# Kernel tuning notes

Measured on AMD Instinct MI355X. Metric: run time of the kernel, lower is better.

Reference implementation:

```python
import jax, jax.numpy as jnp
import numpy as np

EPS = 1e-5
N, A, CTX, H, E = 100000, 32, 5, 64, 1600000


def layer_norm(x, g, b):
    mu = x.mean(-1, keepdims=True)
    var = x.var(-1, keepdims=True)
    return (x - mu) / jnp.sqrt(var + EPS) * g + b


def batch_norm(x, g, b, m, v):
    # eval-mode BatchNorm with running stats
    return (x - m) / jnp.sqrt(v + EPS) * g + b


def gcn_conv(x, w, bias, src, dst, n):
    # src/dst already include self-loops; symmetric normalization D^-1/2 (A+I) D^-1/2
    h = x @ w
    deg = jax.ops.segment_sum(jnp.ones_like(src, dtype=x.dtype), dst, num_segments=n)
    inv_sqrt = jnp.where(deg > 0, 1.0 / jnp.sqrt(deg), 0.0)
    coef = inv_sqrt[src] * inv_sqrt[dst]  # [Etot]
    return jax.ops.segment_sum(h[src] * coef[:, None], dst, num_segments=n) + bias


def gat_conv(x, w, a_src, a_dst, bias, src, dst, n, heads, out_ch):
    h = (x @ w).reshape(n, heads, out_ch)           # [N,H,C]
    alpha_s = (h * a_src).sum(-1)                    # [N,H]
    alpha_d = (h * a_dst).sum(-1)                    # [N,H]
    e = jax.nn.leaky_relu(alpha_s[src] + alpha_d[dst], 0.2)  # [Etot,H]
    m = jax.ops.segment_max(e, dst, num_segments=n)  # segment softmax over incoming edges
    ex = jnp.exp(e - m[dst])
    s = jax.ops.segment_sum(ex, dst, num_segments=n)
    alpha = ex / (s[dst] + 1e-16)                    # [Etot,H]
    out = jax.ops.segment_sum(h[src] * alpha[..., None], dst, num_segments=n)
    return out.reshape(n, heads * out_ch) + bias


def setup_inputs() -> dict:
    key = jax.random.key(0)
    ks = iter(jax.random.split(key, 48))

    def rn(shape, scale=None):
        if scale is None:  # xavier-normal-ish
            fan_in, fan_out = (shape[0], shape[-1]) if len(shape) > 1 else (shape[0], shape[0])
            scale = float(np.sqrt(2.0 / (fan_in + fan_out)))
        return jax.random.normal(next(ks), shape, jnp.float32) * scale

    inp = {
        "accessibility_features": jax.random.normal(next(ks), (N, A), jnp.float32),
        "context_features": jax.random.normal(next(ks), (N, CTX), jnp.float32),
        "edge_index": jax.random.randint(next(ks), (2, E), 0, N, jnp.int32),
        # context gate
        "cg_w1": rn((CTX, 32)), "cg_b1": jnp.zeros((32,), jnp.float32),
        "cg_w2": rn((32, 32)), "cg_b2": jnp.zeros((32,), jnp.float32),
        "cg_aw": rn((32, A)), "cg_ab": jnp.zeros((A,), jnp.float32),
        "base_imp": jnp.ones((A,), jnp.float32),
        # input LayerNorm
        "ln_g": jnp.ones((A,), jnp.float32), "ln_b": jnp.zeros((A,), jnp.float32),
        # feature encoder
        "fe_w1": rn((A, H)), "fe_b1": jnp.zeros((H,), jnp.float32),
        "fe_w2": rn((H, H)), "fe_b2": jnp.zeros((H,), jnp.float32),
        # GCN1 + BN1
        "gcn1_w": rn((H, H)), "gcn1_b": jnp.zeros((H,), jnp.float32),
        "bn1_g": 1.0 + rn((H,), 0.05), "bn1_b": rn((H,), 0.05),
        "bn1_m": rn((H,), 0.05), "bn1_v": 1.0 + jax.random.uniform(next(ks), (H,), jnp.float32) * 0.1,
        # GAT (heads=2, out=32) + BN2
        "gat_w": rn((H, H)), "gat_asrc": rn((2, 32), 0.1), "gat_adst": rn((2, 32), 0.1),
        "gat_b": jnp.zeros((H,), jnp.float32),
        "bn2_g": 1.0 + rn((H,), 0.05), "bn2_b": rn((H,), 0.05),
        "bn2_m": rn((H,), 0.05), "bn2_v": 1.0 + jax.random.uniform(next(ks), (H,), jnp.float32) * 0.1,
        # GCN2 + BN3
        "gcn2_w": rn((H, H // 2)), "gcn2_b": jnp.zeros((H // 2,), jnp.float32),
        "bn3_g": 1.0 + rn((H // 2,), 0.05), "bn3_b": rn((H // 2,), 0.05),
        "bn3_m": rn((H // 2,), 0.05), "bn3_v": 1.0 + jax.random.uniform(next(ks), (H // 2,), jnp.float32) * 0.1,
        # SVI predictor head
        "sp_w1": rn((H // 2, H // 4)), "sp_b1": jnp.zeros((H // 4,), jnp.float32),
        "sp_w2": rn((H // 4, 1)), "sp_b2": jnp.zeros((1,), jnp.float32),
    }
    return inp


def reference(accessibility_features, context_features, edge_index,
              cg_w1, cg_b1, cg_w2, cg_b2, cg_aw, cg_ab, base_imp,
              ln_g, ln_b, fe_w1, fe_b1, fe_w2, fe_b2,
              gcn1_w, gcn1_b, bn1_g, bn1_b, bn1_m, bn1_v,
              gat_w, gat_asrc, gat_adst, gat_b, bn2_g, bn2_b, bn2_m, bn2_v,
              gcn2_w, gcn2_b, bn3_g, bn3_b, bn3_m, bn3_v,
              sp_w1, sp_b1, sp_w2, sp_b2):
    n = accessibility_features.shape[0]
    loops = jnp.arange(n, dtype=edge_index.dtype)
    src = jnp.concatenate([edge_index[0], loops])
    dst = jnp.concatenate([edge_index[1], loops])

    # context-gated feature modulation
    ce = jax.nn.relu(context_features @ cg_w1 + cg_b1) @ cg_w2 + cg_b2
    attw = jax.nn.softmax(ce @ cg_aw + cg_ab, axis=-1)
    x = layer_norm(accessibility_features * (attw * base_imp), ln_g, ln_b)

    # dense feature encoder (dropout = identity in eval)
    x = jax.nn.relu(jax.nn.relu(x @ fe_w1 + fe_b1) @ fe_w2 + fe_b2)

    x = jax.nn.relu(batch_norm(gcn_conv(x, gcn1_w, gcn1_b, src, dst, n), bn1_g, bn1_b, bn1_m, bn1_v))
    x = jax.nn.relu(batch_norm(gat_conv(x, gat_w, gat_asrc, gat_adst, gat_b, src, dst, n, 2, 32), bn2_g, bn2_b, bn2_m, bn2_v))
    x = jax.nn.relu(batch_norm(gcn_conv(x, gcn2_w, gcn2_b, src, dst, n), bn3_g, bn3_b, bn3_m, bn3_v))

    svi = jax.nn.sigmoid((jax.nn.relu(x @ sp_w1 + sp_b1) @ sp_w2 + sp_b2).squeeze(-1))
    return svi
```

## Files before the change

### kernel.cpp

```cpp
#include <hip/hip_runtime.h>
#include <hip/hip_bf16.h>

constexpr int A_DIM = 32;
constexpr int CTX_DIM = 5;
constexpr float EPS = 1e-5f;
constexpr int BCAP = 4096;

__device__ __forceinline__ float lrelu02(float x) { return x > 0.f ? x : 0.2f * x; }

__device__ __forceinline__ unsigned int f2bf_bits(float x) {
    __hip_bfloat16 h = __float2bfloat16(x);
    return (unsigned int)reinterpret_cast<unsigned short&>(h);
}
__device__ __forceinline__ float bf_lo(unsigned int v) { return __uint_as_float(v << 16); }
__device__ __forceinline__ float bf_hi(unsigned int v) { return __uint_as_float(v & 0xffff0000u); }

__global__ void k_bucketA(const int* __restrict__ ei, int E, int* __restrict__ bcnt,
                          int* __restrict__ bstage) {
    int i = blockIdx.x * blockDim.x + threadIdx.x;
    int e4 = E >> 2;
    const int4* s4 = (const int4*)ei;
    const int4* d4 = (const int4*)(ei + E);
    auto put = [&](int s, int d) {
        int b = d >> 7;
        int pos = atomicAdd(&bcnt[b * 16], 1);
        if (pos < BCAP) bstage[(size_t)b * BCAP + pos] = ((d & 127) << 17) | s;
    };
    if (i < e4) {
        int4 s = s4[i];
        int4 d = d4[i];
        put(s.x, d.x);
        put(s.y, d.y);
        put(s.z, d.z);
        put(s.w, d.w);
    }
    int tb = e4 << 2;
    if (i < E - tb) put(ei[tb + i], ei[E + tb + i]);
}

__global__ void k_bscan(const int* __restrict__ bcnt, int nb, int* __restrict__ bbase,
                        int* __restrict__ rowp, int n, int E) {
    __shared__ int sd[256];
    int tid = threadIdx.x;
    int run = 0;
    for (int base = 0; base < nb; base += 256) {
        int idx = base + tid;
        int v = (idx < nb) ? min(bcnt[idx * 16], BCAP) : 0;
        sd[tid] = v;
        __syncthreads();
        for (int off = 1; off < 256; off <<= 1) {
            int t = (tid >= off) ? sd[tid - off] : 0;
            __syncthreads();
            sd[tid] += t;
            __syncthreads();
        }
        if (idx < nb) bbase[idx] = run + sd[tid] - v;
        run += sd[255];
        __syncthreads();
    }
    if (tid == 0) rowp[n] = run;
}

__global__ __launch_bounds__(256) void k_bucketB(
    const int* __restrict__ bstage, const int* __restrict__ bcnt, const int* __restrict__ bbase,
    int* __restrict__ rowp, float* __restrict__ inv, int* __restrict__ csrc, int n) {
    __shared__ int scur[128];
    __shared__ int sstage[BCAP];
    int b = blockIdx.x, tid = threadIdx.x;
    int base_node = b << 7;
    int nn = min(128, n - base_node);
    int cntE = min(bcnt[b * 16], BCAP);
    int ebase = bbase[b];
    const int* st = bstage + (size_t)b * BCAP;
    if (tid < 128) scur[tid] = 0;
    __syncthreads();
    for (int i = tid; i < cntE; i += 256) atomicAdd(&scur[st[i] >> 17], 1);
    __syncthreads();
    int deg = (tid < 128) ? scur[tid] : 0;
    __syncthreads();
    if (tid < 128) scur[tid] = deg;
    __syncthreads();
    for (int off = 1; off < 128; off <<= 1) {
        int t = (tid >= off && tid < 128) ? scur[tid - off] : 0;
        __syncthreads();
        if (tid < 128) scur[tid] += t;
        __syncthreads();
    }
    int excl = (tid < 128) ? (scur[tid] - deg) : 0;
    if (tid < nn) {
        rowp[base_node + tid] = ebase + excl;
        inv[base_node + tid] = rsqrtf((float)deg + 1.0f);
    }
    if (tid < 128) scur[tid] = excl;
    __syncthreads();
    for (int i = tid; i < cntE; i += 256) {
        int p = st[i];
        int pos = atomicAdd(&scur[p >> 17], 1);
        sstage[pos] = p & 0x1FFFF;
    }
    __syncthreads();
    for (int i = tid; i < cntE; i += 256) csrc[ebase + i] = sstage[i];
}

__global__ __launch_bounds__(256) void k_gate_encode(
    const float* __restrict__ accf, const float* __restrict__ ctxf,
    const float* __restrict__ w1, const float* __restrict__ b1,
    const float* __restrict__ w2, const float* __restrict__ b2,
    const float* __restrict__ aw, const float* __restrict__ ab,
    const float* __restrict__ base_imp, const float* __restrict__ lng,
    const float* __restrict__ lnb, const float* __restrict__ fw1,
    const float* __restrict__ fb1, const float* __restrict__ fw2,
    const float* __restrict__ fb2, float* __restrict__ xout, int n) {
    __shared__ float sh[4][128];
    int tid = threadIdx.x, wid = tid >> 6, lane = tid & 63;
    int l = lane & 31, half = lane >> 5;
    float w1c[CTX_DIM], w2c[32], awc[32], f1c[32], f2c[64];
#pragma unroll
    for (int k = 0; k < CTX_DIM; k++) w1c[k] = w1[k * 32 + l];
#pragma unroll
    for (int k = 0; k < 32; k++) w2c[k] = w2[k * 32 + l];
#pragma unroll
    for (int k = 0; k < 32; k++) awc[k] = aw[k * 32 + l];
#pragma unroll
    for (int k = 0; k < 32; k++) f1c[k] = fw1[k * 64 + lane];
#pragma unroll
    for (int k = 0; k < 64; k++) f2c[k] = fw2[k * 64 + lane];
    float b1v = b1[l], b2v = b2[l], abv = ab[l], bimp = base_imp[l];
    float lngv = lng[l], lnbv = lnb[l], fb1v = fb1[lane], fb2v = fb2[lane];
    float* s0 = sh[wid];

    int npairs = (n + 1) >> 1;
    int gw = blockIdx.x * 4 + wid, nw = gridDim.x * 4;
    for (int pair = gw; pair < npairs; pair += nw) {
        int node = pair * 2 + half;
        bool valid = node < n;
        float cx0 = 0, cx1 = 0, cx2 = 0, cx3 = 0, cx4 = 0, xa = 0;
        if (valid) {
            cx0 = ctxf[node * CTX_DIM + 0];
            cx1 = ctxf[node * CTX_DIM + 1];
            cx2 = ctxf[node * CTX_DIM + 2];
            cx3 = ctxf[node * CTX_DIM + 3];
            cx4 = ctxf[node * CTX_DIM + 4];
            xa = accf[node * A_DIM + l];
        }
        float h1 = b1v + cx0 * w1c[0] + cx1 * w1c[1] + cx2 * w1c[2] + cx3 * w1c[3] + cx4 * w1c[4];
        h1 = fmaxf(h1, 0.f);
        s0[lane] = h1;
        {
            float a0 = 0, a1 = 0, a2 = 0, a3 = 0;
#pragma unroll
            for (int k = 0; k < 32; k += 4) {
                a0 += s0[half * 32 + k] * w2c[k];
                a1 += s0[half * 32 + k + 1] * w2c[k + 1];
                a2 += s0[half * 32 + k + 2] * w2c[k + 2];
                a3 += s0[half * 32 + k + 3] * w2c[k + 3];
            }
            s0[lane] = b2v + ((a0 + a1) + (a2 + a3));
        }
        float z;
        {
            float a0 = 0, a1 = 0, a2 = 0, a3 = 0;
#pragma unroll
            for (int k = 0; k < 32; k += 4) {
                a0 += s0[half * 32 + k] * awc[k];
                a1 += s0[half * 32 + k + 1] * awc[k + 1];
                a2 += s0[half * 32 + k + 2] * awc[k + 2];
                a3 += s0[half * 32 + k + 3] * awc[k + 3];
            }
            z = abv + ((a0 + a1) + (a2 + a3));
        }
        float m = z;
#pragma unroll
        for (int off = 16; off; off >>= 1) m = fmaxf(m, __shfl_xor(m, off, 64));
        float ex = __expf(z - m);
        float ss = ex;
#pragma unroll
        for (int off = 16; off; off >>= 1) ss += __shfl_xor(ss, off, 64);
        float v = xa * (ex / ss) * bimp;
        float s1 = v, s2 = v * v;
#pragma unroll
        for (int off = 16; off; off >>= 1) {
            s1 += __shfl_xor(s1, off, 64);
            s2 += __shfl_xor(s2, off, 64);
        }
        float mu = s1 * (1.f / 32.f);
        float var = s2 * (1.f / 32.f) - mu * mu;
        float xn = (v - mu) * rsqrtf(var + EPS) * lngv + lnbv;
        s0[lane] = xn;
        float u0, u1;
        {
            float a0 = 0, a1 = 0, b0 = 0, b1a = 0;
#pragma unroll
            for (int k = 0; k < 32; k += 2) {
                a0 += s0[k] * f1c[k];
                a1 += s0[k + 1] * f1c[k + 1];
                b0 += s0[32 + k] * f1c[k];
                b1a += s0[32 + k + 1] * f1c[k + 1];
            }
            u0 = fmaxf(fb1v + a0 + a1, 0.f);
            u1 = fmaxf(fb1v + b0 + b1a, 0.f);
        }
        s0[lane] = u0;
        s0[64 + lane] = u1;
        float o0, o1;
        {
            float a0 = 0, a1 = 0, b0 = 0, b1a = 0;
#pragma unroll
            for (int k = 0; k < 64; k += 2) {
                a0 += s0[k] * f2c[k];
                a1 += s0[k + 1] * f2c[k + 1];
                b0 += s0[64 + k] * f2c[k];
                b1a += s0[64 + k + 1] * f2c[k + 1];
            }
            o0 = fmaxf(fb2v + a0 + a1, 0.f);
            o1 = fmaxf(fb2v + b0 + b1a, 0.f);
        }
        int n0 = pair * 2;
        xout[(size_t)n0 * 64 + lane] = o0;
        if (n0 + 1 < n) xout[(size_t)(n0 + 1) * 64 + lane] = o1;
    }
}

template <int COUT, bool DO_ATTN, bool SCALE>
__global__ __launch_bounds__(256) void k_transform(
    const float* __restrict__ x, const float* __restrict__ w,
    const float* __restrict__ asrc, const float* __restrict__ adst,
    const float* __restrict__ inv, __hip_bfloat16* __restrict__ h,
    float* __restrict__ attn, int n) {
    constexpr int NPG = 64 / COUT;
    __shared__ __align__(16) float scr[4][NPG * 64];
    int tid = threadIdx.x, wid = tid >> 6, lane = tid & 63;
    int ch = lane % COUT;
    int sub = lane / COUT;
    float wr[64];
#pragma unroll
    for (int k = 0; k < 64; k++) wr[k] = w[k * COUT + ch];
    float as_r = 0.f, ad_r = 0.f;
    if (DO_ATTN) {
        as_r = asrc[lane];
        ad_r = adst[lane];
    }
    int ngroups = (n + NPG - 1) / NPG;
    int gw = blockIdx.x * 4 + wid, nw = gridDim.x * 4;
    int total = n * 64;
    unsigned int* h2 = (unsigned int*)h;
    for (int g = gw; g < ngroups; g += nw) {
        int base = g * NPG * 64;
#pragma unroll
        for (int i = 0; i < NPG; i++) {
            int idx = i * 64 + lane;
            scr[wid][idx] = (base + idx < total) ? x[base + idx] : 0.f;
        }
        float acc = 0.f;
        const float* sp = &scr[wid][sub * 64];
#pragma unroll
        for (int k = 0; k < 64; k++) acc += sp[k] * wr[k];
        int node = g * NPG + sub;
        if (SCALE) acc *= (node < n) ? inv[node] : 0.f;
        unsigned int mine = f2bf_bits(acc);
        unsigned int oth = (unsigned int)__shfl_xor((int)mine, 1, 64);
        if ((ch & 1) == 0 && node < n)
            h2[(size_t)node * (COUT / 2) + (ch >> 1)] = mine | (oth << 16);
        if (DO_ATTN) {
            float ps = acc * as_r, pd = acc * ad_r;
#pragma unroll
            for (int off = 16; off; off >>= 1) {
                ps += __shfl_xor(ps, off, 64);
                pd += __shfl_xor(pd, off, 64);
            }
            if ((lane & 31) == 0 && node < n) {
                int hd = lane >> 5;
                attn[node * 4 + hd] = ps;
                attn[node * 4 + 2 + hd] = pd;
            }
        }
    }
}

template <int C>
__global__ __launch_bounds__(256) void k_gcn_agg(
    const __hip_bfloat16* __restrict__ h, const int* __restrict__ rowp,
    const int* __restrict__ csrc, const float* __restrict__ inv,
    const float* __restrict__ bias, const float* __restrict__ bg,
    const float* __restrict__ bb, const float* __restrict__ bm,
    const float* __restrict__ bv, float* __restrict__ out, int n) {
    constexpr int LPE = C / 2;
    constexpr int NE = 64 / LPE;
    int tid = threadIdx.x, lane = tid & 63;
    int node = blockIdx.x * 4 + (tid >> 6);
    if (node >= n) return;
    float invd = inv[node];
    int e0 = rowp[node], e1 = rowp[node + 1];
    int l = lane & (LPE - 1);
    int grp = lane / LPE;
    const unsigned int* h2 = (const unsigned int*)h;
    float acc0 = 0.f, acc1 = 0.f;
    for (int cb = e0; cb < e1; cb += 64) {
        int kn = min(64, e1 - cb);
        int s_l = (lane < kn) ? csrc[cb + lane] : node;
        for (int kb = 0; kb < kn; kb += NE * 8) {
            unsigned int v[8];
            float msk[8];
#pragma unroll
            for (int i = 0; i < 8; i++) {
                int k = kb + i * NE + grp;
                int s = __shfl(s_l, k, 64);
                msk[i] = (k < kn) ? 1.f : 0.f;
                v[i] = h2[(size_t)s * LPE + l];
            }
#pragma unroll
            for (int i = 0; i < 8; i++) {
                acc0 += msk[i] * bf_lo(v[i]);
                acc1 += msk[i] * bf_hi(v[i]);
            }
        }
    }
#pragma unroll
    for (int off = LPE; off < 64; off <<= 1) {
        acc0 += __shfl_xor(acc0, off, 64);
        acc1 += __shfl_xor(acc1, off, 64);
    }
    unsigned int sv = h2[(size_t)node * LPE + l];
    acc0 = (acc0 + bf_lo(sv)) * invd;
    acc1 = (acc1 + bf_hi(sv)) * invd;
    if (grp == 0) {
        int c0 = 2 * l;
        float sc0 = bg[c0] * rsqrtf(bv[c0] + EPS);
        float sc1 = bg[c0 + 1] * rsqrtf(bv[c0 + 1] + EPS);
        float r0 = (acc0 + bias[c0] - bm[c0]) * sc0 + bb[c0];
        float r1 = (acc1 + bias[c0 + 1] - bm[c0 + 1]) * sc1 + bb[c0 + 1];
        ((float2*)out)[(size_t)node * LPE + l] = make_float2(fmaxf(r0, 0.f), fmaxf(r1, 0.f));
    }
}

__global__ __launch_bounds__(256) void k_gat_agg(
    const __hip_bfloat16* __restrict__ h, const int* __restrict__ rowp,
    const int* __restrict__ csrc, const float* __restrict__ attn,
    const float* __restrict__ bias, const float* __restrict__ bg,
    const float* __restrict__ bb, const float* __restrict__ bm,
    const float* __restrict__ bv, float* __restrict__ out, int n) {
    __shared__ uint2 sed[4][64];
    int tid = threadIdx.x, lane = tid & 63, wid = tid >> 6;
    int node = blockIdx.x * 4 + wid;
    if (node >= n) return;
    uint2* se = sed[wid];
    const float4* a4p = (const float4*)attn;
    float4 ad = a4p[node];
    float ad0 = ad.z, ad1 = ad.w;
    float es0 = lrelu02(ad.x + ad0), es1 = lrelu02(ad.y + ad1);
    int e0 = rowp[node], e1 = rowp[node + 1];
    int deg = e1 - e0;
    int kn0 = min(deg, 64);
    int s_l = (lane < kn0) ? csrc[e0 + lane] : node;
    float4 a_l = a4p[s_l];
    float l0 = (lane < kn0) ? lrelu02(a_l.x + ad0) : -3.4e38f;
    float l1 = (lane < kn0) ? lrelu02(a_l.y + ad1) : -3.4e38f;
    float m0 = fmaxf(l0, es0), m1 = fmaxf(l1, es1);
    for (int cb = e0 + 64; cb < e1; cb += 64) {
        if (cb + lane < e1) {
            float4 a = a4p[csrc[cb + lane]];
            m0 = fmaxf(m0, lrelu02(a.x + ad0));
            m1 = fmaxf(m1, lrelu02(a.y + ad1));
        }
    }
#pragma unroll
    for (int off = 32; off; off >>= 1) {
        m0 = fmaxf(m0, __shfl_xor(m0, off, 64));
        m1 = fmaxf(m1, __shfl_xor(m1, off, 64));
    }
    float ex0 = (lane < kn0) ? __expf(l0 - m0) : 0.f;
    float ex1 = (lane < kn0) ? __expf(l1 - m1) : 0.f;
    float t0 = ex0, t1 = ex1;
    se[lane] = make_uint2((unsigned int)s_l, f2bf_bits(ex0) | (f2bf_bits(ex1) << 16));
    int l = lane & 31, grp = lane >> 5;
    bool hd2 = l >= 16;
    const unsigned int* h2 = (const unsigned int*)h;
    float acc0 = 0.f, acc1 = 0.f;
    for (int kb = 0; kb < kn0; kb += 16) {
        unsigned int v[8];
        float wg[8];
#pragma unroll
        for (int i = 0; i < 8; i++) {
            int k = kb + i * 2 + grp;
            uint2 e = se[k];
            wg[i] = hd2 ? bf_hi(e.y) : bf_lo(e.y);
            v[i] = h2[(size_t)e.x * 32 + l];
        }
#pragma unroll
        for (int i = 0; i < 8; i++) {
            acc0 += wg[i] * bf_lo(v[i]);
            acc1 += wg[i] * bf_hi(v[i]);
        }
    }
    for (int cb = e0 + 64; cb < e1; cb += 64) {
        int kn = min(64, e1 - cb);
        int s_c = (lane < kn) ? csrc[cb + lane] : node;
        float4 a_c = a4p[s_c];
        float c0 = (lane < kn) ? __expf(lrelu02(a_c.x + ad0) - m0) : 0.f;
        float c1 = (lane < kn) ? __expf(lrelu02(a_c.y + ad1) - m1) : 0.f;
        t0 += c0;
        t1 += c1;
        se[lane] = make_uint2((unsigned int)s_c, f2bf_bits(c0) | (f2bf_bits(c1) << 16));
        for (int kb = 0; kb < kn; kb += 16) {
            unsigned int v[8];
            float wg[8];
#pragma unroll
            for (int i = 0; i < 8; i++) {
                int k = kb + i * 2 + grp;
                uint2 e = se[k];
                wg[i] = hd2 ? bf_hi(e.y) : bf_lo(e.y);
                v[i] = h2[(size_t)e.x * 32 + l];
            }
#pragma unroll
            for (int i = 0; i < 8; i++) {
                acc0 += wg[i] * bf_lo(v[i]);
                acc1 += wg[i] * bf_hi(v[i]);
            }
        }
    }
#pragma unroll
    for (int off = 32; off; off >>= 1) {
        t0 += __shfl_xor(t0, off, 64);
        t1 += __shfl_xor(t1, off, 64);
    }
    t0 += __expf(es0 - m0);
    t1 += __expf(es1 - m1);
    acc0 += __shfl_xor(acc0, 32, 64);
    acc1 += __shfl_xor(acc1, 32, 64);
    unsigned int sv = h2[(size_t)node * 32 + l];
    float ws = hd2 ? __expf(es1 - m1) : __expf(es0 - m0);
    acc0 += ws * bf_lo(sv);
    acc1 += ws * bf_hi(sv);
    float rsh = hd2 ? (1.f / (t1 + 1e-16f)) : (1.f / (t0 + 1e-16f));
    acc0 *= rsh;
    acc1 *= rsh;
    if (grp == 0) {
        int c0 = 2 * l;
        float sc0 = bg[c0] * rsqrtf(bv[c0] + EPS);
        float sc1 = bg[c0 + 1] * rsqrtf(bv[c0 + 1] + EPS);
        float r0 = (acc0 + bias[c0] - bm[c0]) * sc0 + bb[c0];
        float r1 = (acc1 + bias[c0 + 1] - bm[c0 + 1]) * sc1 + bb[c0 + 1];
        ((float2*)out)[(size_t)node * 32 + l] = make_float2(fmaxf(r0, 0.f), fmaxf(r1, 0.f));
    }
}

__global__ __launch_bounds__(256) void k_head(
    const float* __restrict__ x, const float* __restrict__ w1, const float* __restrict__ b1,
    const float* __restrict__ w2, const float* __restrict__ b2, float* __restrict__ out, int n) {
    __shared__ float sw1[512], sb1[16], sw2[16];
    __shared__ float sb2v;
    __shared__ float scr[4][64];
    int tid = threadIdx.x;
    for (int i = tid; i < 512; i += 256) sw1[i] = w1[i];
    if (tid < 16) {
        sb1[tid] = b1[tid];
        sw2[tid] = w2[tid];
    }
    if (tid == 0) sb2v = b2[0];
    __syncthreads();
    int wid = tid >> 6, lane = tid & 63;
    int half = lane >> 5;
    int np = (n + 1) >> 1;
    int gw = blockIdx.x * 4 + wid, nw = gridDim.x * 4;
    int total = n * 32;
    for (int g = gw; g < np; g += nw) {
        int idx = g * 64 + lane;
        scr[wid][lane] = (idx < total) ? x[idx] : 0.f;
        int j = lane & 15;
        float u = sb1[j];
#pragma unroll
        for (int k = 0; k < 32; k++) u += scr[wid][half * 32 + k] * sw1[k * 16 + j];
        u = fmaxf(u, 0.f);
        float p = u * sw2[j];
#pragma unroll
        for (int off = 8; off; off >>= 1) p += __shfl_xor(p, off, 64);
        int node = g * 2 + half;
        if ((lane & 31) == 0 && node < n) {
            float z = p + sb2v;
            out[node] = 1.f / (1.f + __expf(-z));
        }
    }
}

extern "C" void kernel_launch(void* const* d_in, const int* in_sizes, int n_in,
                              void* d_out, int out_size, void* d_ws, size_t ws_size,
                              hipStream_t stream) {
    const float* accf = (const float*)d_in[0];
    const float* ctxf = (const float*)d_in[1];
    const int* ei = (const int*)d_in[2];
    const float* cg_w1 = (const float*)d_in[3];
    const float* cg_b1 = (const float*)d_in[4];
    const float* cg_w2 = (const float*)d_in[5];
    const float* cg_b2 = (const float*)d_in[6];
    const float* cg_aw = (const float*)d_in[7];
    const float* cg_ab = (const float*)d_in[8];
    const float* base_imp = (const float*)d_in[9];
    const float* ln_g = (const float*)d_in[10];
    const float* ln_b = (const float*)d_in[11];
    const float* fe_w1 = (const float*)d_in[12];
    const float* fe_b1 = (const float*)d_in[13];
    const float* fe_w2 = (const float*)d_in[14];
    const float* fe_b2 = (const float*)d_in[15];
    const float* gcn1_w = (const float*)d_in[16];
    const float* gcn1_b = (const float*)d_in[17];
    const float* bn1_g = (const float*)d_in[18];
    const float* bn1_b = (const float*)d_in[19];
    const float* bn1_m = (const float*)d_in[20];
    const float* bn1_v = (const float*)d_in[21];
    const float* gat_w = (const float*)d_in[22];
    const float* gat_asrc = (const float*)d_in[23];
    const float* gat_adst = (const float*)d_in[24];
    const float* gat_b = (const float*)d_in[25];
    const float* bn2_g = (const float*)d_in[26];
    const float* bn2_b = (const float*)d_in[27];
    const float* bn2_m = (const float*)d_in[28];
    const float* bn2_v = (const float*)d_in[29];
    const float* gcn2_w = (const float*)d_in[30];
    const float* gcn2_b = (const float*)d_in[31];
    const float* bn3_g = (const float*)d_in[32];
    const float* bn3_b = (const float*)d_in[33];
    const float* bn3_m = (const float*)d_in[34];
    const float* bn3_v = (const float*)d_in[35];
    const float* sp_w1 = (const float*)d_in[36];
    const float* sp_b1 = (const float*)d_in[37];
    const float* sp_w2 = (const float*)d_in[38];
    const float* sp_b2 = (const float*)d_in[39];

    int n = in_sizes[0] / A_DIM;
    int E = in_sizes[2] / 2;
    int NB = (n + 127) >> 7;

    char* p = (char*)d_ws;
    auto alloc = [&](size_t bytes) -> void* {
        void* r = (void*)p;
        p += (bytes + 255) & ~(size_t)255;
        return r;
    };
    float* X = (float*)alloc((size_t)n * 64 * 4);
    __hip_bfloat16* Hb = (__hip_bfloat16*)alloc((size_t)n * 64 * 2);
    float* attn = (float*)alloc((size_t)n * 4 * 4);
    int* rowp = (int*)alloc((size_t)(n + 1) * 4);
    float* inv = (float*)alloc((size_t)n * 4);
    int* csrc = (int*)alloc((size_t)E * 4);
    int* bcnt = (int*)alloc((size_t)NB * 16 * 4);
    int* bbase = (int*)alloc((size_t)NB * 4);
    int* bstage = (int*)alloc((size_t)NB * BCAP * 4);

    const int TB = 256;
    hipMemsetAsync(bcnt, 0, (size_t)NB * 16 * 4, stream);
    k_bucketA<<<((E >> 2) + TB - 1) / TB, TB, 0, stream>>>(ei, E, bcnt, bstage);
    k_bscan<<<1, 256, 0, stream>>>(bcnt, NB, bbase, rowp, n, E);
    k_bucketB<<<NB, 256, 0, stream>>>(bstage, bcnt, bbase, rowp, inv, csrc, n);

    k_gate_encode<<<1024, 256, 0, stream>>>(accf, ctxf, cg_w1, cg_b1, cg_w2, cg_b2, cg_aw, cg_ab,
                                            base_imp, ln_g, ln_b, fe_w1, fe_b1, fe_w2, fe_b2, X, n);
    k_transform<64, false, true><<<1024, 256, 0, stream>>>(X, gcn1_w, nullptr, nullptr, inv, Hb,
                                                           nullptr, n);
    k_gcn_agg<64><<<(n + 3) / 4, 256, 0, stream>>>(Hb, rowp, csrc, inv, gcn1_b, bn1_g, bn1_b,
                                                   bn1_m, bn1_v, X, n);
    k_transform<64, true, false><<<1024, 256, 0, stream>>>(X, gat_w, gat_asrc, gat_adst, nullptr,
                                                           Hb, attn, n);
    k_gat_agg<<<(n + 3) / 4, 256, 0, stream>>>(Hb, rowp, csrc, attn, gat_b, bn2_g, bn2_b, bn2_m,
                                               bn2_v, X, n);
    k_transform<32, false, true><<<1024, 256, 0, stream>>>(X, gcn2_w, nullptr, nullptr, inv, Hb,
                                                           nullptr, n);
    k_gcn_agg<32><<<(n + 3) / 4, 256, 0, stream>>>(Hb, rowp, csrc, inv, gcn2_b, bn3_g, bn3_b,
                                                   bn3_m, bn3_v, X, n);
    k_head<<<512, 256, 0, stream>>>(X, sp_w1, sp_b1, sp_w2, sp_b2, (float*)d_out, n);
}
```

Baseline: 413.4 us.

## Use block-local shared-memory counting sort in edge bucketing to cut global atomics

Each block now takes a chunk of edges and builds a shared-memory histogram of destination buckets. It scans that histogram and scatters the edges into a local staging array. It then reserves space per bucket with one global atomic and copies the packed edges out. This replaces one contended global atomic per edge with one per bucket per block. The costs are heavy shared-memory use, fewer blocks, and serial per-bucket copy loops with scattered writes.

```diff
diff --git a/kernel.cpp b/kernel.cpp
--- a/kernel.cpp
+++ b/kernel.cpp
@@ -5,6 +5,8 @@
 constexpr int CTX_DIM = 5;
 constexpr float EPS = 1e-5f;
 constexpr int BCAP = 4096;
+constexpr int EPB = 8192;
+constexpr int NBP = 800;
 
 __device__ __forceinline__ float lrelu02(float x) { return x > 0.f ? x : 0.2f * x; }
 
@@ -15,27 +17,69 @@
 __device__ __forceinline__ float bf_lo(unsigned int v) { return __uint_as_float(v << 16); }
 __device__ __forceinline__ float bf_hi(unsigned int v) { return __uint_as_float(v & 0xffff0000u); }
 
-__global__ void k_bucketA(const int* __restrict__ ei, int E, int* __restrict__ bcnt,
-                          int* __restrict__ bstage) {
-    int i = blockIdx.x * blockDim.x + threadIdx.x;
-    int e4 = E >> 2;
-    const int4* s4 = (const int4*)ei;
-    const int4* d4 = (const int4*)(ei + E);
-    auto put = [&](int s, int d) {
+__global__ __launch_bounds__(256) void k_bucketA(const int* __restrict__ ei, int E,
+                                                 int* __restrict__ bcnt,
+                                                 int* __restrict__ bstage, int NB) {
+    __shared__ int hist[NBP];
+    __shared__ int hexcl[NBP];
+    __shared__ int cur[NBP];
+    __shared__ int sd[256];
+    __shared__ int stg[EPB];
+    int tid = threadIdx.x;
+    int base = blockIdx.x * EPB;
+    int cnt = min(EPB, E - base);
+    if (cnt <= 0) return;
+    for (int i = tid; i < NBP; i += 256) hist[i] = 0;
+    __syncthreads();
+    for (int i = tid; i < cnt; i += 256) atomicAdd(&hist[ei[E + base + i] >> 7], 1);
+    __syncthreads();
+    {
+        int idx0 = tid * 4;
+        int v[4];
+        int s = 0;
+#pragma unroll
+        for (int j = 0; j < 4; j++) {
+            int idx = idx0 + j;
+            v[j] = (idx < NB) ? hist[idx] : 0;
+            s += v[j];
+        }
+        sd[tid] = s;
+        __syncthreads();
+        for (int off = 1; off < 256; off <<= 1) {
+            int t = (tid >= off) ? sd[tid - off] : 0;
+            __syncthreads();
+            sd[tid] += t;
+            __syncthreads();
+        }
+        int run = tid ? sd[tid - 1] : 0;
+#pragma unroll
+        for (int j = 0; j < 4; j++) {
+            int idx = idx0 + j;
+            if (idx < NBP) {
+                hexcl[idx] = run;
+                cur[idx] = run;
+            }
+            run += v[j];
+        }
+    }
+    __syncthreads();
+    for (int i = tid; i < cnt; i += 256) {
+        int s = ei[base + i];
+        int d = ei[E + base + i];
         int b = d >> 7;
-        int pos = atomicAdd(&bcnt[b * 16], 1);
-        if (pos < BCAP) bstage[(size_t)b * BCAP + pos] = ((d & 127) << 17) | s;
-    };
-    if (i < e4) {
-        int4 s = s4[i];
-        int4 d = d4[i];
-        put(s.x, d.x);
-        put(s.y, d.y);
-        put(s.z, d.z);
-        put(s.w, d.w);
-    }
-    int tb = e4 << 2;
-    if (i < E - tb) put(ei[tb + i], ei[E + tb + i]);
+        int pos = atomicAdd(&cur[b], 1);
+        stg[pos] = ((d & 127) << 17) | s;
+    }
+    __syncthreads();
+    for (int b = tid; b < NB; b += 256) {
+        int c = hist[b];
+        if (!c) continue;
+        int gpos = atomicAdd(&bcnt[b * 16], c);
+        int lim = min(c, BCAP - gpos);
+        int lb = hexcl[b];
+        int* dstp = bstage + (size_t)b * BCAP + gpos;
+        for (int j = 0; j < lim; j++) dstp[j] = stg[lb + j];
+    }
 }
 
 __global__ void k_bscan(const int* __restrict__ bcnt, int nb, int* __restrict__ bbase,
@@ -546,9 +590,8 @@
     int* bbase = (int*)alloc((size_t)NB * 4);
     int* bstage = (int*)alloc((size_t)NB * BCAP * 4);
 
-    const int TB = 256;
     hipMemsetAsync(bcnt, 0, (size_t)NB * 16 * 4, stream);
-    k_bucketA<<<((E >> 2) + TB - 1) / TB, TB, 0, stream>>>(ei, E, bcnt, bstage);
+    k_bucketA<<<(E + EPB - 1) / EPB, 256, 0, stream>>>(ei, E, bcnt, bstage, NB);
     k_bscan<<<1, 256, 0, stream>>>(bcnt, NB, bbase, rowp, n, E);
     k_bucketB<<<NB, 256, 0, stream>>>(bstage, bcnt, bbase, rowp, inv, csrc, n);
 
```

Result: faster. 349.5 us (-15.5%).
